# Kernel tuning notes

Measured on AMD Instinct MI355X. Metric: run time of the kernel, lower is better.

The kernel has to match this reference:

```python
import jax, jax.numpy as jnp
import numpy as np

TEMP = 0.1
GROUPS = 16
EPS = 1e-5
COS_EPS = 1e-8


def _encoder(x, conv_w, conv_b, gn_g, gn_b):
    # Conv2d(C,C,3,pad=1) -> GroupNorm(16,C) -> ReLU -> AdaptiveAvgPool2d(1) -> Flatten
    y = jax.lax.conv_general_dilated(
        x, conv_w, window_strides=(1, 1), padding='SAME',
        dimension_numbers=('NCHW', 'OIHW', 'NCHW')) + conv_b[None, :, None, None]
    B, C, H, W = y.shape
    yg = y.reshape(B, GROUPS, C // GROUPS, H, W)
    mu = yg.mean(axis=(2, 3, 4), keepdims=True)
    var = yg.var(axis=(2, 3, 4), keepdims=True)
    yn = ((yg - mu) * jax.lax.rsqrt(var + EPS)).reshape(B, C, H, W)
    y = yn * gn_g[None, :, None, None] + gn_b[None, :, None, None]
    y = jax.nn.relu(y)
    return y.mean(axis=(2, 3))  # [B, C]


def _projector(h, w1, b1, w2, b2, ln_g, ln_b):
    h = jax.nn.relu(h @ w1 + b1)
    h = h @ w2 + b2
    mu = h.mean(axis=-1, keepdims=True)
    var = h.var(axis=-1, keepdims=True)
    return (h - mu) * jax.lax.rsqrt(var + EPS) * ln_g + ln_b


def _predictor(z, w1, b1, w2, b2):
    return jax.nn.relu(z @ w1 + b1) @ w2 + b2


def _l2norm(z):
    n = jnp.sqrt(jnp.sum(z * z, axis=1, keepdims=True))
    return z / jnp.maximum(n, COS_EPS)


def _pair_loss(zi, zj, off_idx):
    # vectorized version of the nested-loop cosine-sim + cross-entropy (label 0)
    S = (_l2norm(zi) @ _l2norm(zj).T) / TEMP  # [B, B]
    pos = jnp.diagonal(S)                     # sim(i_k, j_k)
    neg = jnp.take_along_axis(S, off_idx, axis=1)  # [B, B-1], row k = S[k, l!=k]
    logits = jnp.concatenate([pos[:, None], neg], axis=1)
    return jnp.mean(jax.nn.logsumexp(logits, axis=1) - logits[:, 0])


def setup_inputs() -> dict:
    key = jax.random.key(0)
    ks = jax.random.split(key, 32)
    B, C, H, W, P = 256, 256, 16, 16, 128
    d = {}
    d['x_t2w'] = jax.random.normal(ks[0], (B, C, H, W), jnp.float32)
    d['x_t2f'] = jax.random.normal(ks[1], (B, C, H, W), jnp.float32)
    d['x_t1n'] = jax.random.normal(ks[2], (B, C, H, W), jnp.float32)
    i = 3
    for m in ('t2w', 't2f', 't1n'):
        d[f'conv_w_{m}'] = jax.random.normal(ks[i], (C, C, 3, 3), jnp.float32) * 0.02; i += 1
        d[f'conv_b_{m}'] = jnp.zeros((C,), jnp.float32)
        d[f'gn_g_{m}'] = jnp.ones((C,), jnp.float32)
        d[f'gn_b_{m}'] = jnp.zeros((C,), jnp.float32)
    d['proj_w1'] = jax.random.normal(ks[i], (C, C), jnp.float32) * 0.02; i += 1
    d['proj_b1'] = jnp.zeros((C,), jnp.float32)
    d['proj_w2'] = jax.random.normal(ks[i], (C, P), jnp.float32) * 0.02; i += 1
    d['proj_b2'] = jnp.zeros((P,), jnp.float32)
    d['ln_g'] = jnp.ones((P,), jnp.float32)
    d['ln_b'] = jnp.zeros((P,), jnp.float32)
    d['pred_w1'] = jax.random.normal(ks[i], (P, P), jnp.float32) * 0.02; i += 1
    d['pred_b1'] = jnp.zeros((P,), jnp.float32)
    d['pred_w2'] = jax.random.normal(ks[i], (P, P), jnp.float32) * 0.02; i += 1
    d['pred_b2'] = jnp.zeros((P,), jnp.float32)
    return d


def reference(x_t2w, x_t2f, x_t1n,
              conv_w_t2w, conv_b_t2w, gn_g_t2w, gn_b_t2w,
              conv_w_t2f, conv_b_t2f, gn_g_t2f, gn_b_t2f,
              conv_w_t1n, conv_b_t1n, gn_g_t1n, gn_b_t1n,
              proj_w1, proj_b1, proj_w2, proj_b2, ln_g, ln_b,
              pred_w1, pred_b1, pred_w2, pred_b2):
    xs = [x_t2w, x_t2f, x_t1n]
    enc_params = [(conv_w_t2w, conv_b_t2w, gn_g_t2w, gn_b_t2w),
                  (conv_w_t2f, conv_b_t2f, gn_g_t2f, gn_b_t2f),
                  (conv_w_t1n, conv_b_t1n, gn_g_t1n, gn_b_t1n)]
    encoded = [_encoder(x, *p) for x, p in zip(xs, enc_params)]
    projected = [_projector(e, proj_w1, proj_b1, proj_w2, proj_b2, ln_g, ln_b) for e in encoded]
    preds = [_predictor(z, pred_w1, pred_b1, pred_w2, pred_b2) for z in projected]

    B = projected[0].shape[0]
    off_idx = jnp.asarray(np.array([[l for l in range(B) if l != k] for k in range(B)],
                                    dtype=np.int32))
    pairs = [(0, 1), (0, 2), (1, 2)]
    loss = sum(_pair_loss(projected[i], projected[j], off_idx) for i, j in pairs) / len(pairs)

    return (jnp.stack(encoded), jnp.stack(projected), jnp.stack(preds), loss)
```

## Files before the change

### kernel.cpp

```cpp
#include <hip/hip_runtime.h>
#include <hip/hip_bf16.h>

typedef float f32x4 __attribute__((ext_vector_type(4)));
typedef __bf16 bf16x8 __attribute__((ext_vector_type(8)));
typedef unsigned short u16x8 __attribute__((ext_vector_type(8)));

#define GN_EPS 1e-5f
#define LN_EPS 1e-5f
#define COS_EPS_F 1e-8f

__device__ __forceinline__ unsigned short f2bf(float f) {
  unsigned int u = __builtin_bit_cast(unsigned int, f);
  u += 0x7fffu + ((u >> 16) & 1u);
  return (unsigned short)(u >> 16);
}

__global__ void transpose_kernel(const float* __restrict__ x0,
                                 const float* __restrict__ x1,
                                 const float* __restrict__ x2,
                                 unsigned short* __restrict__ xT,
                                 unsigned int strideElems, int mBase) {
  __shared__ float lds[64][129];
  int m = mBase + (blockIdx.x >> 11);
  int bid = blockIdx.x & 2047;
  const float* x = (m == 0) ? x0 : ((m == 1) ? x1 : x2);
  unsigned short* dst = xT + (unsigned int)(m - mBase) * strideElems;

  int hwt = bid & 3, cit = (bid >> 2) & 1, b = bid >> 3;
  int hw0 = hwt * 64, ci0 = cit * 128;
  int tid = threadIdx.x;

  int hwx = tid & 63, cy0 = tid >> 6;
  const float* xb = x + (b * 256 + ci0) * 256 + hw0;
  #pragma unroll 8
  for (int p = 0; p < 32; ++p) {
    int cy = cy0 + 4 * p;
    lds[hwx][cy] = xb[cy * 256 + hwx];
  }
  __syncthreads();

  int cp = tid & 63, hy0 = tid >> 6;
  unsigned int* outp = (unsigned int*)(dst + (b * 256 + hw0) * 256 + ci0);
  #pragma unroll 4
  for (int p = 0; p < 16; ++p) {
    int hy = hy0 + 4 * p;
    float lo = lds[hy][2 * cp];
    float hi = lds[hy][2 * cp + 1];
    unsigned int w = ((unsigned int)f2bf(hi) << 16) | f2bf(lo);
    outp[hy * 128 + cp] = w;
  }
}

__global__ void pack_kernel(const float* __restrict__ w0,
                            const float* __restrict__ w1,
                            const float* __restrict__ w2,
                            unsigned short* __restrict__ wp,
                            unsigned short* __restrict__ zerobuf) {
  int m = blockIdx.y;
  const float* w = (m == 0) ? w0 : ((m == 1) ? w1 : w2);
  int idx = blockIdx.x * 256 + threadIdx.x;
  if (m == 0 && blockIdx.x == 0) zerobuf[threadIdx.x] = 0;
  int ci = idx & 255;
  int rest = idx >> 8;
  int khw = rest % 9, co = rest / 9;
  wp[m * 589824 + idx] = f2bf(w[(co * 256 + ci) * 9 + khw]);
}

__device__ __forceinline__ void gl_lds16(const unsigned short* g, unsigned short* l) {
  __builtin_amdgcn_global_load_lds(
      (const __attribute__((address_space(1))) void*)g,
      (__attribute__((address_space(3))) void*)l, 16, 0, 0);
}

__launch_bounds__(512, 2)
__global__ void conv_gn_pool(const unsigned short* __restrict__ xT,
                             unsigned int xTstride,
                             const unsigned short* __restrict__ wp,
                             const unsigned short* __restrict__ zb,
                             const float* __restrict__ cb0, const float* __restrict__ cb1,
                             const float* __restrict__ cb2,
                             const float* __restrict__ gg0, const float* __restrict__ gg1,
                             const float* __restrict__ gg2,
                             const float* __restrict__ gb0, const float* __restrict__ gb1,
                             const float* __restrict__ gb2,
                             float* __restrict__ enc, int mBase) {
  __shared__ unsigned short Ab[4][8192];
  __shared__ unsigned short Bb[4][8192];
  __shared__ float gsum[16], gsq[16], pooled[256];

  int mm = mBase + (blockIdx.x >> 8);
  int bb = blockIdx.x & 255;
  int b = (bb & 7) * 32 + (bb >> 3);
  const float* cbias = (mm == 0) ? cb0 : ((mm == 1) ? cb1 : cb2);
  const float* gng   = (mm == 0) ? gg0 : ((mm == 1) ? gg1 : gg2);
  const float* gnb   = (mm == 0) ? gb0 : ((mm == 1) ? gb1 : gb2);

  int tid = threadIdx.x;
  int wid = tid >> 6, lane = tid & 63;
  int wr = wid >> 2, wc = wid & 3;
  int l15 = lane & 15, l4 = lane >> 4;

  if (tid < 16) { gsum[tid] = 0.f; gsq[tid] = 0.f; }
  if (tid < 256) pooled[tid] = 0.f;

  int s0 = tid, s1 = 512 + tid;
  int r0 = s0 >> 2, c0 = s0 & 3;
  int r1 = s1 >> 2, c1 = s1 & 3;
  int cs0 = (c0 ^ ((r0 >> 1) & 3)) * 8;
  int cs1 = (c1 ^ ((r1 >> 1) & 3)) * 8;
  int rh0 = r0 >> 4, rw0 = r0 & 15;
  int rh1 = r1 >> 4, rw1 = r1 & 15;

  const unsigned short* xb = xT + (unsigned int)(mm - mBase) * xTstride + b * 65536;
  const unsigned short* wpm = wp + mm * 589824;
  const unsigned short* bB0 = wpm + r0 * 2304 + cs0;
  const unsigned short* bB1 = wpm + r1 * 2304 + cs1;

  int kch = (l4 ^ ((l15 >> 1) & 3)) * 8;
  int base_af = (wr * 128 + l15) * 32 + kch;
  int base_bf = (wc * 64 + l15) * 32 + kch;

  f32x4 acc[8][4];
  #pragma unroll
  for (int i = 0; i < 8; ++i)
    #pragma unroll
    for (int j = 0; j < 4; ++j) acc[i][j] = (f32x4)(0.0f);

  int kc3 = 0, kh3 = 0, kw3 = 0;

  #define STAGE(SBUF)                                                          \
    {                                                                          \
      int ci0_ = kc3 * 32;                                                     \
      unsigned short* dstA = &Ab[(SBUF)][0];                                   \
      int h0_ = rh0 + kh3 - 1, w0_ = rw0 + kw3 - 1;                            \
      const unsigned short* sA0 = ((unsigned)h0_ < 16u && (unsigned)w0_ < 16u) \
          ? xb + ((h0_ * 16 + w0_) * 256 + ci0_ + cs0) : zb;                   \
      gl_lds16(sA0, dstA + s0 * 8);                                            \
      int h1_ = rh1 + kh3 - 1, w1_ = rw1 + kw3 - 1;                            \
      const unsigned short* sA1 = ((unsigned)h1_ < 16u && (unsigned)w1_ < 16u) \
          ? xb + ((h1_ * 16 + w1_) * 256 + ci0_ + cs1) : zb;                   \
      gl_lds16(sA1, dstA + s1 * 8);                                            \
      int offB = (kh3 * 3 + kw3) * 256 + ci0_;                                 \
      unsigned short* dstB = &Bb[(SBUF)][0];                                   \
      gl_lds16(bB0 + offB, dstB + s0 * 8);                                     \
      gl_lds16(bB1 + offB, dstB + s1 * 8);                                     \
      kw3 = kw3 + 1; int cw_ = (kw3 == 3); kw3 = cw_ ? 0 : kw3; kh3 += cw_;    \
      int ch_ = (kh3 == 3); kh3 = ch_ ? 0 : kh3; kc3 += ch_;                   \
    }

  #define LD8(P) __builtin_bit_cast(bf16x8, *(const u16x8*)(P))

  bf16x8 afP[8], bfrP[4], afQ[8], bfrQ[4];

  #define READF(AF, BF, BUFI)                                                  \
    {                                                                          \
      const unsigned short* Ap_ = &Ab[(BUFI)][0];                              \
      const unsigned short* Bp_ = &Bb[(BUFI)][0];                              \
      _Pragma("unroll")                                                        \
      for (int j = 0; j < 8; ++j) AF[j] = LD8(&Ap_[base_af + j * 512]);        \
      _Pragma("unroll")                                                        \
      for (int n = 0; n < 4; ++n) BF[n] = LD8(&Bp_[base_bf + n * 512]);        \
    }

  #define MM(AF, BF)                                                           \
    {                                                                          \
      __builtin_amdgcn_s_setprio(1);                                           \
      _Pragma("unroll")                                                        \
      for (int j = 0; j < 8; ++j)                                              \
        _Pragma("unroll")                                                      \
        for (int n = 0; n < 4; ++n)                                            \
          acc[j][n] = __builtin_amdgcn_mfma_f32_16x16x32_bf16(                 \
              AF[j], BF[n], acc[j][n], 0, 0, 0);                               \
      __builtin_amdgcn_s_setprio(0);                                           \
    }

  STAGE(0); STAGE(1);
  asm volatile("s_waitcnt vmcnt(4)" ::: "memory");
  __builtin_amdgcn_s_barrier();
  READF(afP, bfrP, 0);

  for (int t2 = 0; t2 < 35; ++t2) {
    {
      int t = 2 * t2;
      STAGE((t + 2) & 3);
      asm volatile("s_waitcnt vmcnt(4)" ::: "memory");
      __builtin_amdgcn_s_barrier();
      READF(afQ, bfrQ, (t + 1) & 3);
      asm volatile("s_waitcnt lgkmcnt(12)" ::: "memory");
      __builtin_amdgcn_sched_barrier(0);
      MM(afP, bfrP);
    }
    {
      int t = 2 * t2 + 1;
      STAGE((t + 2) & 3);
      asm volatile("s_waitcnt vmcnt(4)" ::: "memory");
      __builtin_amdgcn_s_barrier();
      READF(afP, bfrP, (t + 1) & 3);
      asm volatile("s_waitcnt lgkmcnt(12)" ::: "memory");
      __builtin_amdgcn_sched_barrier(0);
      MM(afQ, bfrQ);
    }
  }
  asm volatile("s_waitcnt vmcnt(0)" ::: "memory");
  __builtin_amdgcn_s_barrier();
  READF(afQ, bfrQ, 3);
  asm volatile("s_waitcnt lgkmcnt(12)" ::: "memory");
  __builtin_amdgcn_sched_barrier(0);
  MM(afP, bfrP);
  asm volatile("s_waitcnt lgkmcnt(0)" ::: "memory");
  __builtin_amdgcn_sched_barrier(0);
  MM(afQ, bfrQ);
  #undef MM
  #undef READF
  #undef STAGE
  #undef LD8

  __syncthreads();

  float bias[4], ggv[4], gbv[4];
  #pragma unroll
  for (int nf = 0; nf < 4; ++nf) {
    int co = wc * 64 + nf * 16 + l15;
    bias[nf] = cbias[co]; ggv[nf] = gng[co]; gbv[nf] = gnb[co];
  }
  #pragma unroll
  for (int nf = 0; nf < 4; ++nf) {
    float s1 = 0.f, s2 = 0.f;
    #pragma unroll
    for (int mf = 0; mf < 8; ++mf)
      #pragma unroll
      for (int i = 0; i < 4; ++i) {
        float v = acc[mf][nf][i] + bias[nf];
        acc[mf][nf][i] = v;
        s1 += v; s2 += v * v;
      }
    #pragma unroll
    for (int d = 1; d < 64; d <<= 1) {
      s1 += __shfl_xor(s1, d);
      s2 += __shfl_xor(s2, d);
    }
    if (lane == 0) {
      atomicAdd(&gsum[wc * 4 + nf], s1);
      atomicAdd(&gsq[wc * 4 + nf], s2);
    }
  }
  __syncthreads();
  #pragma unroll
  for (int nf = 0; nf < 4; ++nf) {
    int g = wc * 4 + nf;
    float mean = gsum[g] * (1.f / 4096.f);
    float var = gsq[g] * (1.f / 4096.f) - mean * mean;
    float rs = rsqrtf(var + GN_EPS);
    float p = 0.f;
    #pragma unroll
    for (int mf = 0; mf < 8; ++mf)
      #pragma unroll
      for (int i = 0; i < 4; ++i) {
        float v = (acc[mf][nf][i] - mean) * rs * ggv[nf] + gbv[nf];
        p += fmaxf(v, 0.f);
      }
    p += __shfl_xor(p, 16);
    p += __shfl_xor(p, 32);
    if (lane < 16) atomicAdd(&pooled[wc * 64 + nf * 16 + l15], p);
  }
  __syncthreads();
  if (tid < 256)
    enc[mm * 65536 + b * 256 + tid] = pooled[tid] * (1.f / 256.f);
}

__global__ void proj_pred(const float* __restrict__ enc,
                          const float* __restrict__ w1, const float* __restrict__ b1,
                          const float* __restrict__ w2, const float* __restrict__ b2,
                          const float* __restrict__ lng, const float* __restrict__ lnb,
                          const float* __restrict__ pw1, const float* __restrict__ pb1,
                          const float* __restrict__ pw2, const float* __restrict__ pb2,
                          float* __restrict__ proj, float* __restrict__ pred,
                          float* __restrict__ znorm) {
  __shared__ float row[256], h1[256], zz[128], p1[128], rbuf[128], red[2];
  int r = blockIdx.x, tid = threadIdx.x;
  row[tid] = enc[r * 256 + tid];
  __syncthreads();
  float a = 0.f;
  for (int k = 0; k < 256; ++k) a += row[k] * w1[k * 256 + tid];
  h1[tid] = fmaxf(a + b1[tid], 0.f);
  __syncthreads();
  if (tid < 128) {
    a = 0.f;
    for (int k = 0; k < 256; ++k) a += h1[k] * w2[k * 128 + tid];
    zz[tid] = a + b2[tid];
  }
  __syncthreads();
  if (tid < 128) rbuf[tid] = zz[tid];
  __syncthreads();
  for (int d = 64; d > 0; d >>= 1) {
    if (tid < d) rbuf[tid] += rbuf[tid + d];
    __syncthreads();
  }
  float mean = rbuf[0] * (1.f / 128.f);
  __syncthreads();
  if (tid < 128) { float dv = zz[tid] - mean; rbuf[tid] = dv * dv; }
  __syncthreads();
  for (int d = 64; d > 0; d >>= 1) {
    if (tid < d) rbuf[tid] += rbuf[tid + d];
    __syncthreads();
  }
  float rstd = rsqrtf(rbuf[0] * (1.f / 128.f) + LN_EPS);
  __syncthreads();
  float zval = 0.f;
  if (tid < 128) {
    zval = (zz[tid] - mean) * rstd * lng[tid] + lnb[tid];
    proj[r * 128 + tid] = zval;
    rbuf[tid] = zval * zval;
  }
  __syncthreads();
  if (tid < 128) zz[tid] = zval;
  for (int d = 64; d > 0; d >>= 1) {
    __syncthreads();
    if (tid < d) rbuf[tid] += rbuf[tid + d];
  }
  __syncthreads();
  float rn = 1.f / fmaxf(sqrtf(rbuf[0]), COS_EPS_F);
  __syncthreads();
  if (tid < 128) {
    znorm[r * 128 + tid] = zz[tid] * rn;
    a = 0.f;
    for (int k = 0; k < 128; ++k) a += zz[k] * pw1[k * 128 + tid];
    p1[tid] = fmaxf(a + pb1[tid], 0.f);
  }
  __syncthreads();
  if (tid < 128) {
    a = 0.f;
// ... 24 lines not shown
  rbuf[tid] = s;
  __syncthreads();
  for (int d = 128; d > 0; d >>= 1) {
    if (tid < d) rbuf[tid] = fmaxf(rbuf[tid], rbuf[tid + d]);
    __syncthreads();
  }
  float m = rbuf[0];
  __syncthreads();
  rbuf[tid] = expf(s - m);
  __syncthreads();
  for (int d = 128; d > 0; d >>= 1) {
    if (tid < d) rbuf[tid] += rbuf[tid + d];
    __syncthreads();
  }
  if (tid == 0) part[blk] = m + logf(rbuf[0]) - sv[k];
}

__global__ void finalize_loss(const float* __restrict__ part, float* __restrict__ out) {
  __shared__ float red[256];
  int tid = threadIdx.x;
  float s = 0.f;
  for (int idx = tid; idx < 768; idx += 256) s += part[idx];
  red[tid] = s;
  __syncthreads();
  for (int d = 128; d > 0; d >>= 1) {
    if (tid < d) red[tid] += red[tid + d];
    __syncthreads();
  }
  if (tid == 0) out[0] = red[0] * (1.f / 768.f);
}

extern "C" void kernel_launch(void* const* d_in, const int* in_sizes, int n_in,
                              void* d_out, int out_size, void* d_ws, size_t ws_size,
                              hipStream_t stream) {
  const float* x[3]  = {(const float*)d_in[0], (const float*)d_in[1], (const float*)d_in[2]};
  const float* cw[3] = {(const float*)d_in[3], (const float*)d_in[7], (const float*)d_in[11]};
  const float* cb[3] = {(const float*)d_in[4], (const float*)d_in[8], (const float*)d_in[12]};
  const float* gg[3] = {(const float*)d_in[5], (const float*)d_in[9], (const float*)d_in[13]};
  const float* gb[3] = {(const float*)d_in[6], (const float*)d_in[10], (const float*)d_in[14]};
  const float* p_w1 = (const float*)d_in[15];
  const float* p_b1 = (const float*)d_in[16];
  const float* p_w2 = (const float*)d_in[17];
  const float* p_b2 = (const float*)d_in[18];
  const float* ln_g = (const float*)d_in[19];
  const float* ln_b = (const float*)d_in[20];
  const float* q_w1 = (const float*)d_in[21];
  const float* q_b1 = (const float*)d_in[22];
  const float* q_w2 = (const float*)d_in[23];
  const float* q_b2 = (const float*)d_in[24];

  float* out = (float*)d_out;
  char* ws = (char*)d_ws;

  const size_t XT_ONE = 33554432;
  bool merged = ws_size >= (3 * XT_ONE + 3538944 + 393216 + 3072 + 512);

  size_t xt_total = merged ? 3 * XT_ONE : XT_ONE;
  unsigned short* xT  = (unsigned short*)ws;
  unsigned short* wpk = (unsigned short*)(ws + xt_total);
  float* znorm = (float*)(ws + xt_total + 3538944);
  float* part  = (float*)(ws + xt_total + 3538944 + 393216);
  unsigned short* zb = (unsigned short*)(ws + xt_total + 3538944 + 393216 + 3072);

  float* enc  = out;
  float* proj = out + 196608;
  float* pred = out + 294912;
  float* lossp = out + 393216;

  pack_kernel<<<dim3(2304, 3), dim3(256), 0, stream>>>(cw[0], cw[1], cw[2], wpk, zb);

  if (merged) {
    transpose_kernel<<<dim3(6144), dim3(256), 0, stream>>>(x[0], x[1], x[2], xT, 16777216u, 0);
    conv_gn_pool<<<dim3(768), dim3(512), 0, stream>>>(
        xT, 16777216u, wpk, zb, cb[0], cb[1], cb[2], gg[0], gg[1], gg[2],
        gb[0], gb[1], gb[2], enc, 0);
  } else {
    for (int m = 0; m < 3; ++m) {
      transpose_kernel<<<dim3(2048), dim3(256), 0, stream>>>(x[0], x[1], x[2], xT, 0u, m);
      conv_gn_pool<<<dim3(256), dim3(512), 0, stream>>>(
          xT, 0u, wpk, zb, cb[0], cb[1], cb[2], gg[0], gg[1], gg[2],
          gb[0], gb[1], gb[2], enc, m);
    }
  }
  proj_pred<<<dim3(768), dim3(256), 0, stream>>>(enc, p_w1, p_b1, p_w2, p_b2, ln_g, ln_b,
                                                 q_w1, q_b1, q_w2, q_b2, proj, pred, znorm);
  loss_kernel<<<dim3(768), dim3(256), 0, stream>>>(znorm, part);
  finalize_loss<<<dim3(1), dim3(256), 0, stream>>>(part, lossp);
}
```

Before: 299.8 us.

## Fuse weight packing into transpose and loop modalities inside persistent conv blocks

Weight packing is folded into the transpose launch as extra blocks, removing a separate kernel launch. The conv+GroupNorm+pool kernel now launches one block per batch sample and loops over the three modalities inside, instead of one block per (modality, sample). This aims to avoid the partial second wave of blocks. It risks lower occupancy (one block per CU instead of two) and less latency hiding.

```diff
diff --git a/kernel.cpp b/kernel.cpp
--- a/kernel.cpp
+++ b/kernel.cpp
@@ -15,20 +15,42 @@
   return (unsigned short)(u >> 16);
 }
 
-__global__ void transpose_kernel(const float* __restrict__ x0,
-                                 const float* __restrict__ x1,
-                                 const float* __restrict__ x2,
-                                 unsigned short* __restrict__ xT,
-                                 unsigned int strideElems, int mBase) {
+__global__ void transpose_pack_kernel(const float* __restrict__ x0,
+                                      const float* __restrict__ x1,
+                                      const float* __restrict__ x2,
+                                      unsigned short* __restrict__ xT,
+                                      unsigned int strideElems, int mBase, int nTrans,
+                                      const float* __restrict__ w0,
+                                      const float* __restrict__ w1,
+                                      const float* __restrict__ w2,
+                                      unsigned short* __restrict__ wp,
+                                      unsigned short* __restrict__ zerobuf,
+                                      int doPack) {
   __shared__ float lds[64][129];
-  int m = mBase + (blockIdx.x >> 11);
-  int bid = blockIdx.x & 2047;
+  int gbid = blockIdx.x;
+  int tid = threadIdx.x;
+
+  if (gbid >= nTrans) {
+    if (!doPack) return;
+    int pb = gbid - nTrans;
+    int m = pb / 2304;
+    int pidx = (pb - m * 2304) * 256 + tid;
+    const float* w = (m == 0) ? w0 : ((m == 1) ? w1 : w2);
+    if (pb == 0) zerobuf[tid] = 0;
+    int ci = pidx & 255;
+    int rest = pidx >> 8;
+    int khw = rest % 9, co = rest / 9;
+    wp[m * 589824 + pidx] = f2bf(w[(co * 256 + ci) * 9 + khw]);
+    return;
+  }
+
+  int m = mBase + (gbid >> 11);
+  int bid = gbid & 2047;
   const float* x = (m == 0) ? x0 : ((m == 1) ? x1 : x2);
   unsigned short* dst = xT + (unsigned int)(m - mBase) * strideElems;
 
   int hwt = bid & 3, cit = (bid >> 2) & 1, b = bid >> 3;
   int hw0 = hwt * 64, ci0 = cit * 128;
-  int tid = threadIdx.x;
 
   int hwx = tid & 63, cy0 = tid >> 6;
   const float* xb = x + (b * 256 + ci0) * 256 + hw0;
@@ -49,21 +71,6 @@
     unsigned int w = ((unsigned int)f2bf(hi) << 16) | f2bf(lo);
     outp[hy * 128 + cp] = w;
   }
-}
-
-__global__ void pack_kernel(const float* __restrict__ w0,
-                            const float* __restrict__ w1,
-                            const float* __restrict__ w2,
-                            unsigned short* __restrict__ wp,
-                            unsigned short* __restrict__ zerobuf) {
-  int m = blockIdx.y;
-  const float* w = (m == 0) ? w0 : ((m == 1) ? w1 : w2);
-  int idx = blockIdx.x * 256 + threadIdx.x;
-  if (m == 0 && blockIdx.x == 0) zerobuf[threadIdx.x] = 0;
-  int ci = idx & 255;
-  int rest = idx >> 8;
-  int khw = rest % 9, co = rest / 9;
-  wp[m * 589824 + idx] = f2bf(w[(co * 256 + ci) * 9 + khw]);
 }
 
 __device__ __forceinline__ void gl_lds16(const unsigned short* g, unsigned short* l) {
@@ -83,25 +90,18 @@
                              const float* __restrict__ gg2,
                              const float* __restrict__ gb0, const float* __restrict__ gb1,
                              const float* __restrict__ gb2,
-                             float* __restrict__ enc, int mBase) {
+                             float* __restrict__ enc, int mBase, int nM) {
   __shared__ unsigned short Ab[4][8192];
   __shared__ unsigned short Bb[4][8192];
   __shared__ float gsum[16], gsq[16], pooled[256];
 
-  int mm = mBase + (blockIdx.x >> 8);
   int bb = blockIdx.x & 255;
   int b = (bb & 7) * 32 + (bb >> 3);
-  const float* cbias = (mm == 0) ? cb0 : ((mm == 1) ? cb1 : cb2);
-  const float* gng   = (mm == 0) ? gg0 : ((mm == 1) ? gg1 : gg2);
-  const float* gnb   = (mm == 0) ? gb0 : ((mm == 1) ? gb1 : gb2);
 
   int tid = threadIdx.x;
   int wid = tid >> 6, lane = tid & 63;
   int wr = wid >> 2, wc = wid & 3;
   int l15 = lane & 15, l4 = lane >> 4;
-
-  if (tid < 16) { gsum[tid] = 0.f; gsq[tid] = 0.f; }
-  if (tid < 256) pooled[tid] = 0.f;
 
   int s0 = tid, s1 = 512 + tid;
   int r0 = s0 >> 2, c0 = s0 & 3;
@@ -111,161 +111,174 @@
   int rh0 = r0 >> 4, rw0 = r0 & 15;
   int rh1 = r1 >> 4, rw1 = r1 & 15;
 
-  const unsigned short* xb = xT + (unsigned int)(mm - mBase) * xTstride + b * 65536;
-  const unsigned short* wpm = wp + mm * 589824;
-  const unsigned short* bB0 = wpm + r0 * 2304 + cs0;
-  const unsigned short* bB1 = wpm + r1 * 2304 + cs1;
-
   int kch = (l4 ^ ((l15 >> 1) & 3)) * 8;
   int base_af = (wr * 128 + l15) * 32 + kch;
   int base_bf = (wc * 64 + l15) * 32 + kch;
 
-  f32x4 acc[8][4];
-  #pragma unroll
-  for (int i = 0; i < 8; ++i)
+  for (int mi = 0; mi < nM; ++mi) {
+    int mm = mBase + mi;
+    const float* cbias = (mm == 0) ? cb0 : ((mm == 1) ? cb1 : cb2);
+    const float* gng   = (mm == 0) ? gg0 : ((mm == 1) ? gg1 : gg2);
+    const float* gnb   = (mm == 0) ? gb0 : ((mm == 1) ? gb1 : gb2);
+
+    if (tid < 16) { gsum[tid] = 0.f; gsq[tid] = 0.f; }
+    if (tid < 256) pooled[tid] = 0.f;
+
+    const unsigned short* xb = xT + (unsigned int)mi * xTstride + b * 65536;
+    const unsigned short* wpm = wp + mm * 589824;
+    const unsigned short* bB0 = wpm + r0 * 2304 + cs0;
+    const unsigned short* bB1 = wpm + r1 * 2304 + cs1;
+
+    f32x4 acc[8][4];
     #pragma unroll
-    for (int j = 0; j < 4; ++j) acc[i][j] = (f32x4)(0.0f);
-
-  int kc3 = 0, kh3 = 0, kw3 = 0;
-
-  #define STAGE(SBUF)                                                          \
-    {                                                                          \
-      int ci0_ = kc3 * 32;                                                     \
-      unsigned short* dstA = &Ab[(SBUF)][0];                                   \
-      int h0_ = rh0 + kh3 - 1, w0_ = rw0 + kw3 - 1;                            \
-      const unsigned short* sA0 = ((unsigned)h0_ < 16u && (unsigned)w0_ < 16u) \
-          ? xb + ((h0_ * 16 + w0_) * 256 + ci0_ + cs0) : zb;                   \
-      gl_lds16(sA0, dstA + s0 * 8);                                            \
-      int h1_ = rh1 + kh3 - 1, w1_ = rw1 + kw3 - 1;                            \
-      const unsigned short* sA1 = ((unsigned)h1_ < 16u && (unsigned)w1_ < 16u) \
-          ? xb + ((h1_ * 16 + w1_) * 256 + ci0_ + cs1) : zb;                   \
-      gl_lds16(sA1, dstA + s1 * 8);                                            \
-      int offB = (kh3 * 3 + kw3) * 256 + ci0_;                                 \
-      unsigned short* dstB = &Bb[(SBUF)][0];                                   \
-      gl_lds16(bB0 + offB, dstB + s0 * 8);                                     \
-      gl_lds16(bB1 + offB, dstB + s1 * 8);                                     \
-      kw3 = kw3 + 1; int cw_ = (kw3 == 3); kw3 = cw_ ? 0 : kw3; kh3 += cw_;    \
-      int ch_ = (kh3 == 3); kh3 = ch_ ? 0 : kh3; kc3 += ch_;                   \
+    for (int i = 0; i < 8; ++i)
+      #pragma unroll
+      for (int j = 0; j < 4; ++j) acc[i][j] = (f32x4)(0.0f);
+
+    int kc3 = 0, kh3 = 0, kw3 = 0;
+
+    #define STAGE(SBUF)                                                        \
+      {                                                                        \
+        int ci0_ = kc3 * 32;                                                   \
+        unsigned short* dstA = &Ab[(SBUF)][0];                                 \
+        int h0_ = rh0 + kh3 - 1, w0_ = rw0 + kw3 - 1;                          \
+        const unsigned short* sA0 =                                            \
+            ((unsigned)h0_ < 16u && (unsigned)w0_ < 16u)                       \
+                ? xb + ((h0_ * 16 + w0_) * 256 + ci0_ + cs0) : zb;             \
+        gl_lds16(sA0, dstA + s0 * 8);                                          \
+        int h1_ = rh1 + kh3 - 1, w1_ = rw1 + kw3 - 1;                          \
+        const unsigned short* sA1 =                                            \
+            ((unsigned)h1_ < 16u && (unsigned)w1_ < 16u)                       \
+                ? xb + ((h1_ * 16 + w1_) * 256 + ci0_ + cs1) : zb;             \
+        gl_lds16(sA1, dstA + s1 * 8);                                          \
+        int offB = (kh3 * 3 + kw3) * 256 + ci0_;                               \
+        unsigned short* dstB = &Bb[(SBUF)][0];                                 \
+        gl_lds16(bB0 + offB, dstB + s0 * 8);                                   \
+        gl_lds16(bB1 + offB, dstB + s1 * 8);                                   \
+        kw3 = kw3 + 1; int cw_ = (kw3 == 3); kw3 = cw_ ? 0 : kw3; kh3 += cw_;  \
+        int ch_ = (kh3 == 3); kh3 = ch_ ? 0 : kh3; kc3 += ch_;                 \
+      }
+
+    #define LD8(P) __builtin_bit_cast(bf16x8, *(const u16x8*)(P))
+
+    bf16x8 afP[8], bfrP[4], afQ[8], bfrQ[4];
+
+    #define READF(AF, BF, BUFI)                                                \
+      {                                                                        \
+        const unsigned short* Ap_ = &Ab[(BUFI)][0];                            \
+        const unsigned short* Bp_ = &Bb[(BUFI)][0];                            \
+        _Pragma("unroll")                                                      \
+        for (int j = 0; j < 8; ++j) AF[j] = LD8(&Ap_[base_af + j * 512]);      \
+        _Pragma("unroll")                                                      \
+        for (int n = 0; n < 4; ++n) BF[n] = LD8(&Bp_[base_bf + n * 512]);      \
+      }
+
+    #define MM(AF, BF)                                                         \
+      {                                                                        \
+        __builtin_amdgcn_s_setprio(1);                                         \
+        _Pragma("unroll")                                                      \
+        for (int j = 0; j < 8; ++j)                                            \
+          _Pragma("unroll")                                                    \
+          for (int n = 0; n < 4; ++n)                                          \
+            acc[j][n] = __builtin_amdgcn_mfma_f32_16x16x32_bf16(               \
+                AF[j], BF[n], acc[j][n], 0, 0, 0);                             \
+        __builtin_amdgcn_s_setprio(0);                                         \
+      }
+
+    STAGE(0); STAGE(1);
+    asm volatile("s_waitcnt vmcnt(4)" ::: "memory");
+    __builtin_amdgcn_s_barrier();
+    READF(afP, bfrP, 0);
+
+    for (int t2 = 0; t2 < 35; ++t2) {
+      {
+        int t = 2 * t2;
+        STAGE((t + 2) & 3);
+        asm volatile("s_waitcnt vmcnt(4)" ::: "memory");
+        __builtin_amdgcn_s_barrier();
+        READF(afQ, bfrQ, (t + 1) & 3);
+        asm volatile("s_waitcnt lgkmcnt(12)" ::: "memory");
+        __builtin_amdgcn_sched_barrier(0);
+        MM(afP, bfrP);
+      }
+      {
+        int t = 2 * t2 + 1;
+        STAGE((t + 2) & 3);
+        asm volatile("s_waitcnt vmcnt(4)" ::: "memory");
+        __builtin_amdgcn_s_barrier();
+        READF(afP, bfrP, (t + 1) & 3);
+        asm volatile("s_waitcnt lgkmcnt(12)" ::: "memory");
+        __builtin_amdgcn_sched_barrier(0);
+        MM(afQ, bfrQ);
+      }
     }
-
-  #define LD8(P) __builtin_bit_cast(bf16x8, *(const u16x8*)(P))
-
-  bf16x8 afP[8], bfrP[4], afQ[8], bfrQ[4];
-
-  #define READF(AF, BF, BUFI)                                                  \
-    {                                                                          \
-      const unsigned short* Ap_ = &Ab[(BUFI)][0];                              \
-      const unsigned short* Bp_ = &Bb[(BUFI)][0];                              \
-      _Pragma("unroll")                                                        \
-      for (int j = 0; j < 8; ++j) AF[j] = LD8(&Ap_[base_af + j * 512]);        \
-      _Pragma("unroll")                                                        \
-      for (int n = 0; n < 4; ++n) BF[n] = LD8(&Bp_[base_bf + n * 512]);        \
+    asm volatile("s_waitcnt vmcnt(0)" ::: "memory");
+    __builtin_amdgcn_s_barrier();
+    READF(afQ, bfrQ, 3);
+    asm volatile("s_waitcnt lgkmcnt(12)" ::: "memory");
+    __builtin_amdgcn_sched_barrier(0);
+    MM(afP, bfrP);
+    asm volatile("s_waitcnt lgkmcnt(0)" ::: "memory");
+    __builtin_amdgcn_sched_barrier(0);
+    MM(afQ, bfrQ);
+    #undef MM
+    #undef READF
+    #undef STAGE
+    #undef LD8
+
+    __syncthreads();
+
+    float bias[4], ggv[4], gbv[4];
+    #pragma unroll
+    for (int nf = 0; nf < 4; ++nf) {
+      int co = wc * 64 + nf * 16 + l15;
+      bias[nf] = cbias[co]; ggv[nf] = gng[co]; gbv[nf] = gnb[co];
     }
-
-  #define MM(AF, BF)                                                           \
-    {                                                                          \
-      __builtin_amdgcn_s_setprio(1);                                           \
-      _Pragma("unroll")                                                        \
-      for (int j = 0; j < 8; ++j)                                              \
-        _Pragma("unroll")                                                      \
-        for (int n = 0; n < 4; ++n)                                            \
-          acc[j][n] = __builtin_amdgcn_mfma_f32_16x16x32_bf16(                 \
-              AF[j], BF[n], acc[j][n], 0, 0, 0);                               \
-      __builtin_amdgcn_s_setprio(0);                                           \
+    #pragma unroll
+    for (int nf = 0; nf < 4; ++nf) {
+      float s1 = 0.f, s2 = 0.f;
+      #pragma unroll
+      for (int mf = 0; mf < 8; ++mf)
+        #pragma unroll
+        for (int i = 0; i < 4; ++i) {
+          float v = acc[mf][nf][i] + bias[nf];
+          acc[mf][nf][i] = v;
+          s1 += v; s2 += v * v;
+        }
+      #pragma unroll
+      for (int d = 1; d < 64; d <<= 1) {
+        s1 += __shfl_xor(s1, d);
+        s2 += __shfl_xor(s2, d);
+      }
+      if (lane == 0) {
+        atomicAdd(&gsum[wc * 4 + nf], s1);
+        atomicAdd(&gsq[wc * 4 + nf], s2);
+      }
     }
-
-  STAGE(0); STAGE(1);
-  asm volatile("s_waitcnt vmcnt(4)" ::: "memory");
-  __builtin_amdgcn_s_barrier();
-  READF(afP, bfrP, 0);
-
-  for (int t2 = 0; t2 < 35; ++t2) {
-    {
-      int t = 2 * t2;
-      STAGE((t + 2) & 3);
-      asm volatile("s_waitcnt vmcnt(4)" ::: "memory");
-      __builtin_amdgcn_s_barrier();
-      READF(afQ, bfrQ, (t + 1) & 3);
-      asm volatile("s_waitcnt lgkmcnt(12)" ::: "memory");
-      __builtin_amdgcn_sched_barrier(0);
-      MM(afP, bfrP);
+    __syncthreads();
+    #pragma unroll
+    for (int nf = 0; nf < 4; ++nf) {
+      int g = wc * 4 + nf;
+      float mean = gsum[g] * (1.f / 4096.f);
+      float var = gsq[g] * (1.f / 4096.f) - mean * mean;
+      float rs = rsqrtf(var + GN_EPS);
+      float p = 0.f;
+      #pragma unroll
+      for (int mf = 0; mf < 8; ++mf)
+        #pragma unroll
+        for (int i = 0; i < 4; ++i) {
+          float v = (acc[mf][nf][i] - mean) * rs * ggv[nf] + gbv[nf];
+          p += fmaxf(v, 0.f);
+        }
+      p += __shfl_xor(p, 16);
+      p += __shfl_xor(p, 32);
+      if (lane < 16) atomicAdd(&pooled[wc * 64 + nf * 16 + l15], p);
     }
-    {
-      int t = 2 * t2 + 1;
-      STAGE((t + 2) & 3);
-      asm volatile("s_waitcnt vmcnt(4)" ::: "memory");
-      __builtin_amdgcn_s_barrier();
-      READF(afP, bfrP, (t + 1) & 3);
-      asm volatile("s_waitcnt lgkmcnt(12)" ::: "memory");
-      __builtin_amdgcn_sched_barrier(0);
-      MM(afQ, bfrQ);
-    }
-  }
-  asm volatile("s_waitcnt vmcnt(0)" ::: "memory");
-  __builtin_amdgcn_s_barrier();
-  READF(afQ, bfrQ, 3);
-  asm volatile("s_waitcnt lgkmcnt(12)" ::: "memory");
-  __builtin_amdgcn_sched_barrier(0);
-  MM(afP, bfrP);
-  asm volatile("s_waitcnt lgkmcnt(0)" ::: "memory");
-  __builtin_amdgcn_sched_barrier(0);
-  MM(afQ, bfrQ);
-  #undef MM
-  #undef READF
-  #undef STAGE
-  #undef LD8
-
-  __syncthreads();
-
-  float bias[4], ggv[4], gbv[4];
-  #pragma unroll
-  for (int nf = 0; nf < 4; ++nf) {
-    int co = wc * 64 + nf * 16 + l15;
-    bias[nf] = cbias[co]; ggv[nf] = gng[co]; gbv[nf] = gnb[co];
-  }
-  #pragma unroll
-  for (int nf = 0; nf < 4; ++nf) {
-    float s1 = 0.f, s2 = 0.f;
-    #pragma unroll
-    for (int mf = 0; mf < 8; ++mf)
-      #pragma unroll
-      for (int i = 0; i < 4; ++i) {
-        float v = acc[mf][nf][i] + bias[nf];
-        acc[mf][nf][i] = v;
-        s1 += v; s2 += v * v;
-      }
-    #pragma unroll
-    for (int d = 1; d < 64; d <<= 1) {
-      s1 += __shfl_xor(s1, d);
-      s2 += __shfl_xor(s2, d);
-    }
-    if (lane == 0) {
-      atomicAdd(&gsum[wc * 4 + nf], s1);
-      atomicAdd(&gsq[wc * 4 + nf], s2);
-    }
-  }
-  __syncthreads();
-  #pragma unroll
-  for (int nf = 0; nf < 4; ++nf) {
-    int g = wc * 4 + nf;
-    float mean = gsum[g] * (1.f / 4096.f);
-    float var = gsq[g] * (1.f / 4096.f) - mean * mean;
-    float rs = rsqrtf(var + GN_EPS);
-    float p = 0.f;
-    #pragma unroll
-    for (int mf = 0; mf < 8; ++mf)
-      #pragma unroll
-      for (int i = 0; i < 4; ++i) {
-        float v = (acc[mf][nf][i] - mean) * rs * ggv[nf] + gbv[nf];
-        p += fmaxf(v, 0.f);
-      }
-    p += __shfl_xor(p, 16);
-    p += __shfl_xor(p, 32);
-    if (lane < 16) atomicAdd(&pooled[wc * 64 + nf * 16 + l15], p);
-  }
-  __syncthreads();
-  if (tid < 256)
-    enc[mm * 65536 + b * 256 + tid] = pooled[tid] * (1.f / 256.f);
+    __syncthreads();
+    if (tid < 256)
+      enc[mm * 65536 + b * 256 + tid] = pooled[tid] * (1.f / 256.f);
+    __syncthreads();
+  }
 }
 
 __global__ void proj_pred(const float* __restrict__ enc,
@@ -276,7 +289,7 @@
                           const float* __restrict__ pw2, const float* __restrict__ pb2,
                           float* __restrict__ proj, float* __restrict__ pred,
                           float* __restrict__ znorm) {
-  __shared__ float row[256], h1[256], zz[128], p1[128], rbuf[128], red[2];
+  __shared__ float row[256], h1[256], zz[128], p1[128], rbuf[128];
   int r = blockIdx.x, tid = threadIdx.x;
   row[tid] = enc[r * 256 + tid];
   __syncthreads();
@@ -422,19 +435,22 @@
   float* pred = out + 294912;
   float* lossp = out + 393216;
 
-  pack_kernel<<<dim3(2304, 3), dim3(256), 0, stream>>>(cw[0], cw[1], cw[2], wpk, zb);
-
   if (merged) {
-    transpose_kernel<<<dim3(6144), dim3(256), 0, stream>>>(x[0], x[1], x[2], xT, 16777216u, 0);
-    conv_gn_pool<<<dim3(768), dim3(512), 0, stream>>>(
+    transpose_pack_kernel<<<dim3(6144 + 6912), dim3(256), 0, stream>>>(
+        x[0], x[1], x[2], xT, 16777216u, 0, 6144,
+        cw[0], cw[1], cw[2], wpk, zb, 1);
+    conv_gn_pool<<<dim3(256), dim3(512), 0, stream>>>(
         xT, 16777216u, wpk, zb, cb[0], cb[1], cb[2], gg[0], gg[1], gg[2],
-        gb[0], gb[1], gb[2], enc, 0);
+        gb[0], gb[1], gb[2], enc, 0, 3);
   } else {
     for (int m = 0; m < 3; ++m) {
-      transpose_kernel<<<dim3(2048), dim3(256), 0, stream>>>(x[0], x[1], x[2], xT, 0u, m);
+      int grid = 2048 + (m == 0 ? 6912 : 0);
+      transpose_pack_kernel<<<dim3(grid), dim3(256), 0, stream>>>(
+          x[0], x[1], x[2], xT, 0u, m, 2048,
+          cw[0], cw[1], cw[2], wpk, zb, (m == 0) ? 1 : 0);
       conv_gn_pool<<<dim3(256), dim3(512), 0, stream>>>(
           xT, 0u, wpk, zb, cb[0], cb[1], cb[2], gg[0], gg[1], gg[2],
-          gb[0], gb[1], gb[2], enc, m);
+          gb[0], gb[1], gb[2], enc, m, 1);
     }
   }
   proj_pred<<<dim3(768), dim3(256), 0, stream>>>(enc, p_w1, p_b1, p_w2, p_b2, ln_g, ln_b,
```

Result: no change. 303.5 us (+1.3%).

## Fuse input transpose into conv kernel with whole-image LDS residency

Applied to the files above, without the earlier changes.

Removes the separate transpose kernel and its bf16 workspace. Each conv block now converts its fp32 image to a swizzled channels-last bf16 copy held entirely in LDS, and then builds the im2col A fragments straight from LDS with masked padding. Only the weights are streamed, through a two-buffer global_load_lds pipeline. Each of 256 blocks loops over the three modalities, which saves the intermediate HBM round trip and a kernel launch. In exchange, the LDS footprint grows to about 160KB per block, so only one block fits per CU, and the image-staging phase is serialized with compute.

```diff
diff --git a/kernel.cpp b/kernel.cpp
--- a/kernel.cpp
+++ b/kernel.cpp
@@ -15,51 +15,13 @@
   return (unsigned short)(u >> 16);
 }
 
-__global__ void transpose_kernel(const float* __restrict__ x0,
-                                 const float* __restrict__ x1,
-                                 const float* __restrict__ x2,
-                                 unsigned short* __restrict__ xT,
-                                 unsigned int strideElems, int mBase) {
-  __shared__ float lds[64][129];
-  int m = mBase + (blockIdx.x >> 11);
-  int bid = blockIdx.x & 2047;
-  const float* x = (m == 0) ? x0 : ((m == 1) ? x1 : x2);
-  unsigned short* dst = xT + (unsigned int)(m - mBase) * strideElems;
-
-  int hwt = bid & 3, cit = (bid >> 2) & 1, b = bid >> 3;
-  int hw0 = hwt * 64, ci0 = cit * 128;
-  int tid = threadIdx.x;
-
-  int hwx = tid & 63, cy0 = tid >> 6;
-  const float* xb = x + (b * 256 + ci0) * 256 + hw0;
-  #pragma unroll 8
-  for (int p = 0; p < 32; ++p) {
-    int cy = cy0 + 4 * p;
-    lds[hwx][cy] = xb[cy * 256 + hwx];
-  }
-  __syncthreads();
-
-  int cp = tid & 63, hy0 = tid >> 6;
-  unsigned int* outp = (unsigned int*)(dst + (b * 256 + hw0) * 256 + ci0);
-  #pragma unroll 4
-  for (int p = 0; p < 16; ++p) {
-    int hy = hy0 + 4 * p;
-    float lo = lds[hy][2 * cp];
-    float hi = lds[hy][2 * cp + 1];
-    unsigned int w = ((unsigned int)f2bf(hi) << 16) | f2bf(lo);
-    outp[hy * 128 + cp] = w;
-  }
-}
-
 __global__ void pack_kernel(const float* __restrict__ w0,
                             const float* __restrict__ w1,
                             const float* __restrict__ w2,
-                            unsigned short* __restrict__ wp,
-                            unsigned short* __restrict__ zerobuf) {
+                            unsigned short* __restrict__ wp) {
   int m = blockIdx.y;
   const float* w = (m == 0) ? w0 : ((m == 1) ? w1 : w2);
   int idx = blockIdx.x * 256 + threadIdx.x;
-  if (m == 0 && blockIdx.x == 0) zerobuf[threadIdx.x] = 0;
   int ci = idx & 255;
   int rest = idx >> 8;
   int khw = rest % 9, co = rest / 9;
@@ -73,199 +35,247 @@
 }
 
 __launch_bounds__(512, 2)
-__global__ void conv_gn_pool(const unsigned short* __restrict__ xT,
-                             unsigned int xTstride,
+__global__ void conv_gn_pool(const float* __restrict__ x0,
+                             const float* __restrict__ x1,
+                             const float* __restrict__ x2,
                              const unsigned short* __restrict__ wp,
-                             const unsigned short* __restrict__ zb,
                              const float* __restrict__ cb0, const float* __restrict__ cb1,
                              const float* __restrict__ cb2,
                              const float* __restrict__ gg0, const float* __restrict__ gg1,
                              const float* __restrict__ gg2,
                              const float* __restrict__ gb0, const float* __restrict__ gb1,
                              const float* __restrict__ gb2,
-                             float* __restrict__ enc, int mBase) {
-  __shared__ unsigned short Ab[4][8192];
-  __shared__ unsigned short Bb[4][8192];
-  __shared__ float gsum[16], gsq[16], pooled[256];
-
-  int mm = mBase + (blockIdx.x >> 8);
+                             float* __restrict__ enc, int nM) {
+  __shared__ unsigned short smem[81920];
+  unsigned short* img = smem;
+  unsigned short* BbP0 = smem + 65536;
+  unsigned short* BbP1 = smem + 73728;
+  const char* imgc = (const char*)smem;
+
   int bb = blockIdx.x & 255;
   int b = (bb & 7) * 32 + (bb >> 3);
-  const float* cbias = (mm == 0) ? cb0 : ((mm == 1) ? cb1 : cb2);
-  const float* gng   = (mm == 0) ? gg0 : ((mm == 1) ? gg1 : gg2);
-  const float* gnb   = (mm == 0) ? gb0 : ((mm == 1) ? gb1 : gb2);
 
   int tid = threadIdx.x;
   int wid = tid >> 6, lane = tid & 63;
   int wr = wid >> 2, wc = wid & 3;
   int l15 = lane & 15, l4 = lane >> 4;
 
-  if (tid < 16) { gsum[tid] = 0.f; gsq[tid] = 0.f; }
-  if (tid < 256) pooled[tid] = 0.f;
-
   int s0 = tid, s1 = 512 + tid;
-  int r0 = s0 >> 2, c0 = s0 & 3;
-  int r1 = s1 >> 2, c1 = s1 & 3;
-  int cs0 = (c0 ^ ((r0 >> 1) & 3)) * 8;
-  int cs1 = (c1 ^ ((r1 >> 1) & 3)) * 8;
-  int rh0 = r0 >> 4, rw0 = r0 & 15;
-  int rh1 = r1 >> 4, rw1 = r1 & 15;
-
-  const unsigned short* xb = xT + (unsigned int)(mm - mBase) * xTstride + b * 65536;
-  const unsigned short* wpm = wp + mm * 589824;
-  const unsigned short* bB0 = wpm + r0 * 2304 + cs0;
-  const unsigned short* bB1 = wpm + r1 * 2304 + cs1;
+  int co0 = s0 >> 2, c0 = s0 & 3;
+  int co1 = s1 >> 2, c1 = s1 & 3;
+  int cs0 = (c0 ^ ((co0 >> 1) & 3)) * 8;
+  int cs1 = (c1 ^ ((co1 >> 1) & 3)) * 8;
 
   int kch = (l4 ^ ((l15 >> 1) & 3)) * 8;
-  int base_af = (wr * 128 + l15) * 32 + kch;
   int base_bf = (wc * 64 + l15) * 32 + kch;
 
-  f32x4 acc[8][4];
-  #pragma unroll
-  for (int i = 0; i < 8; ++i)
+  for (int mm = 0; mm < nM; ++mm) {
+    const float* xs = ((mm == 0) ? x0 : ((mm == 1) ? x1 : x2)) + b * 65536;
+    const float* cbias = (mm == 0) ? cb0 : ((mm == 1) ? cb1 : cb2);
+    const float* gng   = (mm == 0) ? gg0 : ((mm == 1) ? gg1 : gg2);
+    const float* gnb   = (mm == 0) ? gb0 : ((mm == 1) ? gb1 : gb2);
+    const unsigned short* wpm = wp + mm * 589824;
+    const unsigned short* bB0 = wpm + co0 * 2304 + cs0;
+    const unsigned short* bB1 = wpm + co1 * 2304 + cs1;
+
+    {
+      float* scr = (float*)BbP0;
+      for (int st = 0; st < 8; ++st) {
+        for (int pt2 = 0; pt2 < 4; ++pt2) {
+          __syncthreads();
+          #pragma unroll
+          for (int j = 0; j < 4; ++j) {
+            int idx = tid + j * 512;
+            int px = idx & 63, ciL = idx >> 6;
+            scr[px * 33 + ciL] = xs[(st * 32 + ciL) * 256 + pt2 * 64 + px];
+          }
+          __syncthreads();
+          #pragma unroll
+          for (int j = 0; j < 2; ++j) {
+            int k = tid + j * 512;
+            int pxL = k >> 4, cp = k & 15;
+            int pxg = pt2 * 64 + pxL;
+            int ci = st * 32 + cp * 2;
+            float lo = scr[pxL * 33 + cp * 2];
+            float hi = scr[pxL * 33 + cp * 2 + 1];
+            unsigned int wv = ((unsigned int)f2bf(hi) << 16) | f2bf(lo);
+            int cch = ci >> 3;
+            int boff = pxg * 512 + ((cch ^ (pxg & 7)) << 4) + (ci & 7) * 2;
+            *(unsigned int*)((char*)img + boff) = wv;
+          }
+        }
+      }
+      __syncthreads();
+    }
+
+    f32x4 acc[8][4];
     #pragma unroll
-    for (int j = 0; j < 4; ++j) acc[i][j] = (f32x4)(0.0f);
-
-  int kc3 = 0, kh3 = 0, kw3 = 0;
-
-  #define STAGE(SBUF)                                                          \
-    {                                                                          \
-      int ci0_ = kc3 * 32;                                                     \
-      unsigned short* dstA = &Ab[(SBUF)][0];                                   \
-      int h0_ = rh0 + kh3 - 1, w0_ = rw0 + kw3 - 1;                            \
-      const unsigned short* sA0 = ((unsigned)h0_ < 16u && (unsigned)w0_ < 16u) \
-          ? xb + ((h0_ * 16 + w0_) * 256 + ci0_ + cs0) : zb;                   \
-      gl_lds16(sA0, dstA + s0 * 8);                                            \
-      int h1_ = rh1 + kh3 - 1, w1_ = rw1 + kw3 - 1;                            \
-      const unsigned short* sA1 = ((unsigned)h1_ < 16u && (unsigned)w1_ < 16u) \
-          ? xb + ((h1_ * 16 + w1_) * 256 + ci0_ + cs1) : zb;                   \
-      gl_lds16(sA1, dstA + s1 * 8);                                            \
-      int offB = (kh3 * 3 + kw3) * 256 + ci0_;                                 \
-      unsigned short* dstB = &Bb[(SBUF)][0];                                   \
-      gl_lds16(bB0 + offB, dstB + s0 * 8);                                     \
-      gl_lds16(bB1 + offB, dstB + s1 * 8);                                     \
-      kw3 = kw3 + 1; int cw_ = (kw3 == 3); kw3 = cw_ ? 0 : kw3; kh3 += cw_;    \
-      int ch_ = (kh3 == 3); kh3 = ch_ ? 0 : kh3; kc3 += ch_;                   \
-    }
-
-  #define LD8(P) __builtin_bit_cast(bf16x8, *(const u16x8*)(P))
-
-  bf16x8 afP[8], bfrP[4], afQ[8], bfrQ[4];
-
-  #define READF(AF, BF, BUFI)                                                  \
-    {                                                                          \
-      const unsigned short* Ap_ = &Ab[(BUFI)][0];                              \
-      const unsigned short* Bp_ = &Bb[(BUFI)][0];                              \
-      _Pragma("unroll")                                                        \
-      for (int j = 0; j < 8; ++j) AF[j] = LD8(&Ap_[base_af + j * 512]);        \
-      _Pragma("unroll")                                                        \
-      for (int n = 0; n < 4; ++n) BF[n] = LD8(&Bp_[base_bf + n * 512]);        \
-    }
-
-  #define MM(AF, BF)                                                           \
-    {                                                                          \
-      __builtin_amdgcn_s_setprio(1);                                           \
-      _Pragma("unroll")                                                        \
-      for (int j = 0; j < 8; ++j)                                              \
+    for (int i = 0; i < 8; ++i)
+      #pragma unroll
+      for (int j = 0; j < 4; ++j) acc[i][j] = (f32x4)(0.0f);
+
+    int skc = 0, stap = 0;
+    int rkc = 0, rtap = 0;
+    unsigned vmask = 0, s4mask = 0;
+    int obase[8];
+
+    #define UPDB()                                                             \
+      if (rtap < 9) {                                                          \
+        int dh_ = rtap / 3 - 1, dw_ = rtap - (rtap / 3) * 3 - 1;               \
+        unsigned vm_ = 0, sm_ = 0;                                             \
+        _Pragma("unroll")                                                      \
+        for (int mf = 0; mf < 8; ++mf) {                                       \
+          int p_ = wr * 128 + mf * 16 + l15;                                   \
+          int hh_ = (p_ >> 4) + dh_, ww_ = (p_ & 15) + dw_;                    \
+          int pp_ = p_ + dh_ * 16 + dw_;                                       \
+          int ok_ = ((unsigned)hh_ < 16u) && ((unsigned)ww_ < 16u);            \
+          vm_ |= (unsigned)ok_ << mf;                                          \
+          sm_ |= (unsigned)((pp_ >> 2) & 1) << mf;                             \
+          obase[mf] = ok_ ? (pp_ * 512 + ((l4 ^ (pp_ & 3)) << 4)) : 0;         \
+        }                                                                      \
+        vmask = vm_; s4mask = sm_;                                             \
+      }
+
+    #define READF_A(AF)                                                       \
+      {                                                                        \
+        _Pragma("unroll")                                                      \
+        for (int mf = 0; mf < 8; ++mf) {                                       \
+          int ok_ = (int)((vmask >> mf) & 1u);                                 \
+          int s4_ = (int)(((s4mask >> mf) & 1u) << 2);                         \
+          int kct_ = (((rkc << 2) ^ s4_) << 4);                                \
+          int off_ = obase[mf] + (ok_ ? kct_ : 0);                             \
+          u16x8 raw_ = *(const u16x8*)(imgc + off_);                           \
+          u16x8 z_ = {0, 0, 0, 0, 0, 0, 0, 0};                                 \
+          raw_ = ok_ ? raw_ : z_;                                              \
+          AF[mf] = __builtin_bit_cast(bf16x8, raw_);                           \
+        }                                                                      \
+        ++rkc;                                                                 \
+        if (rkc == 8) { rkc = 0; ++rtap; UPDB(); }                             \
+      }
+
+    #define STAGE_B(BUFP)                                                     \
+      {                                                                        \
+        int offB_ = stap * 256 + skc * 32;                                     \
+        gl_lds16(bB0 + offB_, (BUFP) + s0 * 8);                                \
+        gl_lds16(bB1 + offB_, (BUFP) + s1 * 8);                                \
+        ++skc; if (skc == 8) { skc = 0; ++stap; }                              \
+      }
+
+    bf16x8 afP[8], afQ[8], bfr[4];
+
+    #define MM(AF)                                                            \
+      {                                                                        \
+        __builtin_amdgcn_s_setprio(1);                                         \
+        _Pragma("unroll")                                                      \
+        for (int j = 0; j < 8; ++j)                                            \
+          _Pragma("unroll")                                                    \
+          for (int n = 0; n < 4; ++n)                                          \
+            acc[j][n] = __builtin_amdgcn_mfma_f32_16x16x32_bf16(               \
+                AF[j], bfr[n], acc[j][n], 0, 0, 0);                            \
+        __builtin_amdgcn_s_setprio(0);                                         \
+      }
+
+    #define BODY(BSP, BRP, CURA, NXTA, VMN)                                   \
+      {                                                                        \
+        STAGE_B(BSP);                                                          \
+        asm volatile("s_waitcnt vmcnt(" #VMN ")" ::: "memory");                \
+        __builtin_amdgcn_s_barrier();                                          \
         _Pragma("unroll")                                                      \
         for (int n = 0; n < 4; ++n)                                            \
-          acc[j][n] = __builtin_amdgcn_mfma_f32_16x16x32_bf16(                 \
-              AF[j], BF[n], acc[j][n], 0, 0, 0);                               \
-      __builtin_amdgcn_s_setprio(0);                                           \
+          bfr[n] = __builtin_bit_cast(bf16x8,                                  \
+              *(const u16x8*)&(BRP)[base_bf + n * 512]);                       \
+        READF_A(NXTA);                                                         \
+        asm volatile("s_waitcnt lgkmcnt(8)" ::: "memory");                     \
+        __builtin_amdgcn_sched_barrier(0);                                     \
+        MM(CURA);                                                              \
+      }
+
+    UPDB();
+    STAGE_B(BbP0);
+    asm volatile("s_waitcnt vmcnt(0)" ::: "memory");
+    __builtin_amdgcn_s_barrier();
+    READF_A(afP);
+
+    for (int t2 = 0; t2 < 35; ++t2) {
+      BODY(BbP1, BbP0, afP, afQ, 2)
+      BODY(BbP0, BbP1, afQ, afP, 2)
     }
-
-  STAGE(0); STAGE(1);
-  asm volatile("s_waitcnt vmcnt(4)" ::: "memory");
-  __builtin_amdgcn_s_barrier();
-  READF(afP, bfrP, 0);
-
-  for (int t2 = 0; t2 < 35; ++t2) {
-    {
-      int t = 2 * t2;
-      STAGE((t + 2) & 3);
-      asm volatile("s_waitcnt vmcnt(4)" ::: "memory");
-      __builtin_amdgcn_s_barrier();
-      READF(afQ, bfrQ, (t + 1) & 3);
-      asm volatile("s_waitcnt lgkmcnt(12)" ::: "memory");
-      __builtin_amdgcn_sched_barrier(0);
-      MM(afP, bfrP);
+    BODY(BbP1, BbP0, afP, afQ, 2)
+    asm volatile("s_waitcnt vmcnt(0)" ::: "memory");
+    __builtin_amdgcn_s_barrier();
+    #pragma unroll
+    for (int n = 0; n < 4; ++n)
+      bfr[n] = __builtin_bit_cast(bf16x8, *(const u16x8*)&BbP1[base_bf + n * 512]);
+    asm volatile("s_waitcnt lgkmcnt(0)" ::: "memory");
+    __builtin_amdgcn_sched_barrier(0);
+    MM(afQ);
+
+    #undef BODY
+    #undef MM
+    #undef STAGE_B
+    #undef READF_A
+    #undef UPDB
+
+    __syncthreads();
+
+    float* gsum = (float*)BbP0;
+    float* gsq = gsum + 16;
+    float* pooled = gsq + 16;
+    if (tid < 16) { gsum[tid] = 0.f; gsq[tid] = 0.f; }
+    if (tid < 256) pooled[tid] = 0.f;
+    __syncthreads();
+
+    float bias[4], ggv[4], gbv[4];
+    #pragma unroll
+    for (int nf = 0; nf < 4; ++nf) {
+      int co = wc * 64 + nf * 16 + l15;
+      bias[nf] = cbias[co]; ggv[nf] = gng[co]; gbv[nf] = gnb[co];
     }
-    {
-      int t = 2 * t2 + 1;
-      STAGE((t + 2) & 3);
-      asm volatile("s_waitcnt vmcnt(4)" ::: "memory");
-      __builtin_amdgcn_s_barrier();
-      READF(afP, bfrP, (t + 1) & 3);
-      asm volatile("s_waitcnt lgkmcnt(12)" ::: "memory");
-      __builtin_amdgcn_sched_barrier(0);
-      MM(afQ, bfrQ);
+    #pragma unroll
+    for (int nf = 0; nf < 4; ++nf) {
+      float s1v = 0.f, s2v = 0.f;
+      #pragma unroll
+      for (int mf = 0; mf < 8; ++mf)
+        #pragma unroll
+        for (int i = 0; i < 4; ++i) {
+          float v = acc[mf][nf][i] + bias[nf];
+          acc[mf][nf][i] = v;
+          s1v += v; s2v += v * v;
+        }
+      #pragma unroll
+      for (int d = 1; d < 64; d <<= 1) {
+        s1v += __shfl_xor(s1v, d);
+        s2v += __shfl_xor(s2v, d);
+      }
+      if (lane == 0) {
+        atomicAdd(&gsum[wc * 4 + nf], s1v);
+        atomicAdd(&gsq[wc * 4 + nf], s2v);
+      }
     }
-  }
-  asm volatile("s_waitcnt vmcnt(0)" ::: "memory");
-  __builtin_amdgcn_s_barrier();
-  READF(afQ, bfrQ, 3);
-  asm volatile("s_waitcnt lgkmcnt(12)" ::: "memory");
-  __builtin_amdgcn_sched_barrier(0);
-  MM(afP, bfrP);
-  asm volatile("s_waitcnt lgkmcnt(0)" ::: "memory");
-  __builtin_amdgcn_sched_barrier(0);
-  MM(afQ, bfrQ);
-  #undef MM
-  #undef READF
-  #undef STAGE
-  #undef LD8
-
-  __syncthreads();
-
-  float bias[4], ggv[4], gbv[4];
-  #pragma unroll
-  for (int nf = 0; nf < 4; ++nf) {
-    int co = wc * 64 + nf * 16 + l15;
-    bias[nf] = cbias[co]; ggv[nf] = gng[co]; gbv[nf] = gnb[co];
-  }
-  #pragma unroll
-  for (int nf = 0; nf < 4; ++nf) {
-    float s1 = 0.f, s2 = 0.f;
+    __syncthreads();
     #pragma unroll
-    for (int mf = 0; mf < 8; ++mf)
+    for (int nf = 0; nf < 4; ++nf) {
+      int g = wc * 4 + nf;
+      float mean = gsum[g] * (1.f / 4096.f);
+      float var = gsq[g] * (1.f / 4096.f) - mean * mean;
+      float rs = rsqrtf(var + GN_EPS);
+      float p = 0.f;
       #pragma unroll
-      for (int i = 0; i < 4; ++i) {
-        float v = acc[mf][nf][i] + bias[nf];
-        acc[mf][nf][i] = v;
-        s1 += v; s2 += v * v;
-      }
-    #pragma unroll
-    for (int d = 1; d < 64; d <<= 1) {
-      s1 += __shfl_xor(s1, d);
-      s2 += __shfl_xor(s2, d);
+      for (int mf = 0; mf < 8; ++mf)
+        #pragma unroll
+        for (int i = 0; i < 4; ++i) {
+          float v = (acc[mf][nf][i] - mean) * rs * ggv[nf] + gbv[nf];
+          p += fmaxf(v, 0.f);
+        }
+      p += __shfl_xor(p, 16);
+      p += __shfl_xor(p, 32);
+      if (lane < 16) atomicAdd(&pooled[wc * 64 + nf * 16 + l15], p);
     }
-    if (lane == 0) {
-      atomicAdd(&gsum[wc * 4 + nf], s1);
-      atomicAdd(&gsq[wc * 4 + nf], s2);
-    }
-  }
-  __syncthreads();
-  #pragma unroll
-  for (int nf = 0; nf < 4; ++nf) {
-    int g = wc * 4 + nf;
-    float mean = gsum[g] * (1.f / 4096.f);
-    float var = gsq[g] * (1.f / 4096.f) - mean * mean;
-    float rs = rsqrtf(var + GN_EPS);
-    float p = 0.f;
-    #pragma unroll
-    for (int mf = 0; mf < 8; ++mf)
-      #pragma unroll
-      for (int i = 0; i < 4; ++i) {
-        float v = (acc[mf][nf][i] - mean) * rs * ggv[nf] + gbv[nf];
-        p += fmaxf(v, 0.f);
-      }
-    p += __shfl_xor(p, 16);
-    p += __shfl_xor(p, 32);
-    if (lane < 16) atomicAdd(&pooled[wc * 64 + nf * 16 + l15], p);
-  }
-  __syncthreads();
-  if (tid < 256)
-    enc[mm * 65536 + b * 256 + tid] = pooled[tid] * (1.f / 256.f);
+    __syncthreads();
+    if (tid < 256)
+      enc[mm * 65536 + b * 256 + tid] = pooled[tid] * (1.f / 256.f);
+    __syncthreads();
+  }
 }
 
 __global__ void proj_pred(const float* __restrict__ enc,
@@ -276,7 +286,7 @@
                           const float* __restrict__ pw2, const float* __restrict__ pb2,
                           float* __restrict__ proj, float* __restrict__ pred,
                           float* __restrict__ znorm) {
-  __shared__ float row[256], h1[256], zz[128], p1[128], rbuf[128], red[2];
+  __shared__ float row[256], h1[256], zz[128], p1[128], rbuf[128];
   int r = blockIdx.x, tid = threadIdx.x;
   row[tid] = enc[r * 256 + tid];
   __syncthreads();
@@ -407,36 +417,21 @@
   float* out = (float*)d_out;
   char* ws = (char*)d_ws;
 
-  const size_t XT_ONE = 33554432;
-  bool merged = ws_size >= (3 * XT_ONE + 3538944 + 393216 + 3072 + 512);
-
-  size_t xt_total = merged ? 3 * XT_ONE : XT_ONE;
-  unsigned short* xT  = (unsigned short*)ws;
-  unsigned short* wpk = (unsigned short*)(ws + xt_total);
-  float* znorm = (float*)(ws + xt_total + 3538944);
-  float* part  = (float*)(ws + xt_total + 3538944 + 393216);
-  unsigned short* zb = (unsigned short*)(ws + xt_total + 3538944 + 393216 + 3072);
+  unsigned short* wpk = (unsigned short*)ws;
+  float* znorm = (float*)(ws + 3538944);
+  float* part  = (float*)(ws + 3538944 + 393216);
 
   float* enc  = out;
   float* proj = out + 196608;
   float* pred = out + 294912;
   float* lossp = out + 393216;
 
-  pack_kernel<<<dim3(2304, 3), dim3(256), 0, stream>>>(cw[0], cw[1], cw[2], wpk, zb);
-
-  if (merged) {
-    transpose_kernel<<<dim3(6144), dim3(256), 0, stream>>>(x[0], x[1], x[2], xT, 16777216u, 0);
-    conv_gn_pool<<<dim3(768), dim3(512), 0, stream>>>(
-        xT, 16777216u, wpk, zb, cb[0], cb[1], cb[2], gg[0], gg[1], gg[2],
-        gb[0], gb[1], gb[2], enc, 0);
-  } else {
-    for (int m = 0; m < 3; ++m) {
-      transpose_kernel<<<dim3(2048), dim3(256), 0, stream>>>(x[0], x[1], x[2], xT, 0u, m);
-      conv_gn_pool<<<dim3(256), dim3(512), 0, stream>>>(
-          xT, 0u, wpk, zb, cb[0], cb[1], cb[2], gg[0], gg[1], gg[2],
-          gb[0], gb[1], gb[2], enc, m);
-    }
-  }
+  pack_kernel<<<dim3(2304, 3), dim3(256), 0, stream>>>(cw[0], cw[1], cw[2], wpk);
+
+  conv_gn_pool<<<dim3(256), dim3(512), 0, stream>>>(
+      x[0], x[1], x[2], wpk, cb[0], cb[1], cb[2], gg[0], gg[1], gg[2],
+      gb[0], gb[1], gb[2], enc, 3);
+
   proj_pred<<<dim3(768), dim3(256), 0, stream>>>(enc, p_w1, p_b1, p_w2, p_b2, ln_g, ln_b,
                                                  q_w1, q_b1, q_w2, q_b2, proj, pred, znorm);
   loss_kernel<<<dim3(768), dim3(256), 0, stream>>>(znorm, part);
```

Measured after the change: 366.8 us. 22.4% more time.
